# Optimization experiments

Hardware: AMD Instinct MI355X
Metric: run time of the kernel (lower is better)

The kernel has to match this reference:

```python
import jax, jax.numpy as jnp
import numpy as np

B, L, H = 4, 512, 768          # batch, seq_len, bert hidden
S, R = 100, 100                # num candidate spans, num relation pairs
E = 128                        # size embedding dim
TE, TR = 8, 6                  # entity / relation types
MAX_ENT_LEN = 100
NEG = -1e20


def _span_masks(rng, b, n, seq_len, max_len):
    # contiguous span masks with lengths in [1, max_len-1] so sum(-1) < max_len
    starts = rng.integers(0, seq_len - 1, size=(b, n))
    lengths = rng.integers(1, max_len, size=(b, n))
    ends = np.minimum(starts + lengths, seq_len)
    pos = np.arange(seq_len)
    m = (pos[None, None, :] >= starts[..., None]) & (pos[None, None, :] < ends[..., None])
    return jnp.asarray(m.astype(np.int32))


def setup_inputs() -> dict:
    rng = np.random.default_rng(0)
    key = jax.random.key(0)
    k = jax.random.split(key, 6)
    return {
        "last_hidden_state": jax.random.normal(k[0], (B, L, H), jnp.float32),
        "entity_mask": _span_masks(rng, B, S, L, MAX_ENT_LEN),
        "relations": jnp.asarray(rng.integers(0, S, size=(B, R, 2)).astype(np.int32)),
        "relation_context_mask": _span_masks(rng, B, R, L, MAX_ENT_LEN),
        "relation_sample_mask": jnp.asarray(rng.integers(0, 2, size=(B, R)).astype(np.int32)),
        "size_emb": jax.random.normal(k[1], (MAX_ENT_LEN, E), jnp.float32) * 0.02,
        "span_w": jax.random.normal(k[2], (E + 2 * H, TE), jnp.float32) * 0.02,
        "span_b": jnp.zeros((TE,), jnp.float32),
        "rel_w": jax.random.normal(k[3], (2 * E + 3 * H, TR), jnp.float32) * 0.02,
        "rel_b": jnp.zeros((TR,), jnp.float32),
    }


def _masked_max(h, mask):
    # h: [B,L,H], mask: [B,N,L] int {0,1} -> [B,N,H]
    mf = mask[..., None].astype(h.dtype)                       # [B,N,L,1]
    masked = jnp.where(mf == 0, jnp.asarray(NEG, h.dtype), h[:, None] * mf)
    return masked.max(axis=2)


def reference(last_hidden_state, entity_mask, relations, relation_context_mask,
              relation_sample_mask, size_emb, span_w, span_b, rel_w, rel_b):
    b = last_hidden_state.shape[0]
    # ---- entity classification ----
    context = last_hidden_state[:, 0]                          # CLS pooling [B,H]
    entity_size = size_emb[entity_mask.sum(-1)]                # [B,S,E]
    entity = _masked_max(last_hidden_state, entity_mask)       # [B,S,H]
    ctx = jnp.broadcast_to(context[:, None], (b, entity.shape[1], context.shape[-1]))
    entity_repr = jnp.concatenate([entity, ctx, entity_size], axis=-1)
    entity_logit = entity_repr @ span_w + span_b               # [B,S,TE]
    # ---- relation classification ----
    rel_ctx = _masked_max(last_hidden_state, relation_context_mask)  # [B,R,H]
    rel_ctx = jnp.where(relation_sample_mask[..., None] == 1,
                        jnp.zeros((), rel_ctx.dtype), rel_ctx)
    r = relations.shape[1]
    flat = relations.reshape(b, r * 2)                         # [B,2R]
    pair = jnp.take_along_axis(entity, flat[..., None], axis=1).reshape(b, r, -1)      # [B,R,2H]
    pair_size = jnp.take_along_axis(entity_size, flat[..., None], axis=1).reshape(b, r, -1)  # [B,R,2E]
    relation_repr = jnp.concatenate([rel_ctx, pair, pair_size], axis=-1)
    relation_logit = relation_repr @ rel_w + rel_b             # [B,R,TR]
    return entity_logit, relation_logit
```

## Files before the change

kernel.cpp:

```cpp
#include <hip/hip_runtime.h>

#define Bn 4
#define Ln 512
#define Hn 768
#define Sn 100
#define Rn 100
#define En 128
#define TEn 8
#define TRn 6
#define NEGF (-1e20f)
#define CHUNKS 3

__global__ void __launch_bounds__(256)
masked_max_kernel(const float* __restrict__ hid,
                  const int* __restrict__ ent_mask,
                  const int* __restrict__ rel_mask,
                  const int* __restrict__ sample_mask,
                  float* __restrict__ entity,
                  float* __restrict__ relctx,
                  int* __restrict__ entcnt) {
    int blk = blockIdx.x;
    int span_id = blk / CHUNKS;
    int chunk = blk % CHUNKS;
    int b = span_id / (Sn + Rn);
    int idx = span_id % (Sn + Rn);
    bool is_rel = idx >= Sn;
    int span = is_rel ? idx - Sn : idx;

    const int* mask = is_rel ? rel_mask + ((size_t)b * Rn + span) * Ln
                             : ent_mask + ((size_t)b * Sn + span) * Ln;

    __shared__ int pos[Ln];
    __shared__ int cnt_s;
    int tid = threadIdx.x;
    if (tid == 0) cnt_s = 0;
    __syncthreads();
    #pragma unroll
    for (int l = tid; l < Ln; l += 256) {
        if (mask[l] != 0) {
            int p = atomicAdd(&cnt_s, 1);
            pos[p] = l;
        }
    }
    __syncthreads();
    int cnt = cnt_s;

    int d = chunk * 256 + tid;
    const float* hp = hid + (size_t)b * Ln * Hn + d;
    float* out = is_rel ? relctx + ((size_t)b * Rn + span) * Hn
                        : entity + ((size_t)b * Sn + span) * Hn;
    bool zero_out = is_rel && (sample_mask[b * Rn + span] == 1);

    float m = NEGF;
    int i = 0;
    for (; i + 4 <= cnt; i += 4) {
        float v0 = hp[(size_t)pos[i + 0] * Hn];
        float v1 = hp[(size_t)pos[i + 1] * Hn];
        float v2 = hp[(size_t)pos[i + 2] * Hn];
        float v3 = hp[(size_t)pos[i + 3] * Hn];
        m = fmaxf(m, fmaxf(fmaxf(v0, v1), fmaxf(v2, v3)));
    }
    for (; i < cnt; ++i)
        m = fmaxf(m, hp[(size_t)pos[i] * Hn]);

    out[d] = zero_out ? 0.0f : m;
    if (chunk == 0 && !is_rel && tid == 0) entcnt[b * Sn + span] = cnt;
}

template <int NT>
__device__ __forceinline__ void block_reduce_store(float* acc,
                                                   const float* __restrict__ bias,
                                                   float* __restrict__ out_row,
                                                   int tid) {
    #pragma unroll
    for (int t = 0; t < NT; ++t)
        #pragma unroll
        for (int off = 32; off > 0; off >>= 1)
            acc[t] += __shfl_down(acc[t], off, 64);
    __shared__ float red[4][NT];
    int wave = tid >> 6, lane = tid & 63;
    if (lane == 0) {
        #pragma unroll
        for (int t = 0; t < NT; ++t) red[wave][t] = acc[t];
    }
    __syncthreads();
    if (tid < NT) {
        float s = bias[tid];
        #pragma unroll
        for (int w = 0; w < 4; ++w) s += red[w][tid];
        out_row[tid] = s;
    }
}

__global__ void __launch_bounds__(256)
logits_kernel(const float* __restrict__ hid,
              const float* __restrict__ entity,
              const float* __restrict__ relctx,
              const int* __restrict__ relations,
              const int* __restrict__ entcnt,
              const float* __restrict__ size_emb,
              const float* __restrict__ span_w,
              const float* __restrict__ span_b,
              const float* __restrict__ rel_w,
              const float* __restrict__ rel_b,
              float* __restrict__ out_ent,
              float* __restrict__ out_rel) {
    int blk = blockIdx.x;
    int tid = threadIdx.x;

    if (blk < Bn * Sn) {
        int b = blk / Sn;
        const float* ent = entity + (size_t)blk * Hn;
        const float* ctx = hid + (size_t)b * Ln * Hn;
        const float* sz = size_emb + (size_t)entcnt[blk] * En;

        float acc[TEn];
        #pragma unroll
        for (int t = 0; t < TEn; ++t) acc[t] = 0.0f;

        const int K = 2 * Hn + En;
        for (int k = tid; k < K; k += 256) {
            float v;
            if (k < Hn)          v = ent[k];
            else if (k < 2 * Hn) v = ctx[k - Hn];
            else                 v = sz[k - 2 * Hn];
            const float* w = span_w + (size_t)k * TEn;
            #pragma unroll
            for (int t = 0; t < TEn; ++t) acc[t] += v * w[t];
        }
        block_reduce_store<TEn>(acc, span_b, out_ent + (size_t)blk * TEn, tid);
    } else {
        int rblk = blk - Bn * Sn;
        int b = rblk / Rn;
        int a0 = relations[rblk * 2 + 0];
        int a1 = relations[rblk * 2 + 1];
        const float* ctx = relctx + (size_t)rblk * Hn;
        const float* e0 = entity + ((size_t)b * Sn + a0) * Hn;
        const float* e1 = entity + ((size_t)b * Sn + a1) * Hn;
        const float* s0 = size_emb + (size_t)entcnt[b * Sn + a0] * En;
        const float* s1 = size_emb + (size_t)entcnt[b * Sn + a1] * En;

        float acc[TRn];
        #pragma unroll
        for (int t = 0; t < TRn; ++t) acc[t] = 0.0f;

        const int K = 3 * Hn + 2 * En;
        for (int k = tid; k < K; k += 256) {
            float v;
            if (k < Hn)               v = ctx[k];
            else if (k < 2 * Hn)      v = e0[k - Hn];
            else if (k < 3 * Hn)      v = e1[k - 2 * Hn];
            else if (k < 3 * Hn + En) v = s0[k - 3 * Hn];
            else                      v = s1[k - 3 * Hn - En];
            const float* w = rel_w + (size_t)k * TRn;
            #pragma unroll
            for (int t = 0; t < TRn; ++t) acc[t] += v * w[t];
        }
        block_reduce_store<TRn>(acc, rel_b, out_rel + (size_t)rblk * TRn, tid);
    }
}

extern "C" void kernel_launch(void* const* d_in, const int* in_sizes, int n_in,
                              void* d_out, int out_size, void* d_ws, size_t ws_size,
                              hipStream_t stream) {
    const float* hid        = (const float*)d_in[0];
    const int*   ent_mask   = (const int*)d_in[1];
    const int*   relations  = (const int*)d_in[2];
    const int*   rel_mask   = (const int*)d_in[3];
    const int*   samp_mask  = (const int*)d_in[4];
    const float* size_emb   = (const float*)d_in[5];
    const float* span_w     = (const float*)d_in[6];
    const float* span_b     = (const float*)d_in[7];
    const float* rel_w      = (const float*)d_in[8];
    const float* rel_b      = (const float*)d_in[9];

    float* out = (float*)d_out;
    float* out_ent = out;
    float* out_rel = out + Bn * Sn * TEn;

    char* ws = (char*)d_ws;
    float* entity = (float*)ws;
    float* relctx = entity + (size_t)Bn * Sn * Hn;
    int*   entcnt = (int*)(relctx + (size_t)Bn * Rn * Hn);

    masked_max_kernel<<<Bn * (Sn + Rn) * CHUNKS, 256, 0, stream>>>(
        hid, ent_mask, rel_mask, samp_mask, entity, relctx, entcnt);

    logits_kernel<<<Bn * Sn + Bn * Rn, 256, 0, stream>>>(
        hid, entity, relctx, relations, entcnt, size_emb,
        span_w, span_b, rel_w, rel_b, out_ent, out_rel);
}
```

Baseline: 24.26 us.

## Precompute 8-row block maxima and vectorize masked max and logits loads

Adds a pre-pass kernel that computes the max over every aligned 8-row block of the hidden states. The masked-max kernel then combines fully covered blocks from this table and reads individual rows only at span edges, which cuts the number of rows gathered per span. It also uses float4 loads with one 192-thread block per span, and returns early for relation rows whose sample mask zeroes them. The logits kernel switches to vectorized activation and weight loads; the cost is an extra kernel launch and a workspace write.

```diff
diff --git a/kernel.cpp b/kernel.cpp
--- a/kernel.cpp
+++ b/kernel.cpp
@@ -9,62 +9,108 @@
 #define TEn 8
 #define TRn 6
 #define NEGF (-1e20f)
-#define CHUNKS 3
-
-__global__ void __launch_bounds__(256)
+#define W 8
+#define NBLK (Ln / W)
+#define H4 (Hn / 4)
+
+__device__ __forceinline__ float4 fmax4(float4 a, float4 b) {
+    return make_float4(fmaxf(a.x, b.x), fmaxf(a.y, b.y),
+                       fmaxf(a.z, b.z), fmaxf(a.w, b.w));
+}
+
+__global__ void __launch_bounds__(192)
+blockmax_kernel(const float* __restrict__ hid, float* __restrict__ bmax) {
+    int bj = blockIdx.x;
+    int b = bj / NBLK, j = bj % NBLK;
+    int tid = threadIdx.x;
+    const float4* src = (const float4*)(hid + ((size_t)b * Ln + j * W) * Hn);
+    float4 m = src[tid];
+    #pragma unroll
+    for (int r = 1; r < W; ++r)
+        m = fmax4(m, src[(size_t)r * H4 + tid]);
+    ((float4*)(bmax + (size_t)bj * Hn))[tid] = m;
+}
+
+__global__ void __launch_bounds__(192)
 masked_max_kernel(const float* __restrict__ hid,
                   const int* __restrict__ ent_mask,
                   const int* __restrict__ rel_mask,
                   const int* __restrict__ sample_mask,
+                  const float* __restrict__ bmax,
                   float* __restrict__ entity,
                   float* __restrict__ relctx,
                   int* __restrict__ entcnt) {
-    int blk = blockIdx.x;
-    int span_id = blk / CHUNKS;
-    int chunk = blk % CHUNKS;
+    int span_id = blockIdx.x;
     int b = span_id / (Sn + Rn);
     int idx = span_id % (Sn + Rn);
     bool is_rel = idx >= Sn;
     int span = is_rel ? idx - Sn : idx;
+    int tid = threadIdx.x;
+
+    float4* out4 = (float4*)(is_rel ? relctx + ((size_t)b * Rn + span) * Hn
+                                    : entity + ((size_t)b * Sn + span) * Hn);
+
+    if (is_rel && sample_mask[b * Rn + span] == 1) {
+        out4[tid] = make_float4(0.f, 0.f, 0.f, 0.f);
+        return;
+    }
 
     const int* mask = is_rel ? rel_mask + ((size_t)b * Rn + span) * Ln
                              : ent_mask + ((size_t)b * Sn + span) * Ln;
 
-    __shared__ int pos[Ln];
-    __shared__ int cnt_s;
-    int tid = threadIdx.x;
-    if (tid == 0) cnt_s = 0;
+    __shared__ int rows[Ln];
+    __shared__ int blks[NBLK];
+    __shared__ int nrows_s, nblks_s, cnt_s;
+    if (tid == 0) { nrows_s = 0; nblks_s = 0; }
     __syncthreads();
-    #pragma unroll
-    for (int l = tid; l < Ln; l += 256) {
-        if (mask[l] != 0) {
-            int p = atomicAdd(&cnt_s, 1);
-            pos[p] = l;
+
+    int local = 0;
+    if (tid < NBLK) {
+        const int4* m4 = (const int4*)(mask + tid * W);
+        int4 a = m4[0], c = m4[1];
+        int mm[8] = {a.x, a.y, a.z, a.w, c.x, c.y, c.z, c.w};
+        int s = 0;
+        #pragma unroll
+        for (int r = 0; r < 8; ++r) s += (mm[r] != 0);
+        local = s;
+        if (s == 8) {
+            int p = atomicAdd(&nblks_s, 1);
+            blks[p] = tid;
+        } else if (s > 0) {
+            #pragma unroll
+            for (int r = 0; r < 8; ++r)
+                if (mm[r] != 0) { int p = atomicAdd(&nrows_s, 1); rows[p] = tid * W + r; }
         }
+        #pragma unroll
+        for (int off = 32; off > 0; off >>= 1) local += __shfl_down(local, off, 64);
+        if (tid == 0) cnt_s = local;
     }
     __syncthreads();
-    int cnt = cnt_s;
-
-    int d = chunk * 256 + tid;
-    const float* hp = hid + (size_t)b * Ln * Hn + d;
-    float* out = is_rel ? relctx + ((size_t)b * Rn + span) * Hn
-                        : entity + ((size_t)b * Sn + span) * Hn;
-    bool zero_out = is_rel && (sample_mask[b * Rn + span] == 1);
-
-    float m = NEGF;
+    int nrows = nrows_s, nblks = nblks_s, cnt = cnt_s;
+
+    const float4* hb4 = (const float4*)(hid + (size_t)b * Ln * Hn);
+    const float4* bm4 = (const float4*)(bmax + (size_t)b * NBLK * Hn);
+
+    float4 m = make_float4(NEGF, NEGF, NEGF, NEGF);
     int i = 0;
-    for (; i + 4 <= cnt; i += 4) {
-        float v0 = hp[(size_t)pos[i + 0] * Hn];
-        float v1 = hp[(size_t)pos[i + 1] * Hn];
-        float v2 = hp[(size_t)pos[i + 2] * Hn];
-        float v3 = hp[(size_t)pos[i + 3] * Hn];
-        m = fmaxf(m, fmaxf(fmaxf(v0, v1), fmaxf(v2, v3)));
-    }
-    for (; i < cnt; ++i)
-        m = fmaxf(m, hp[(size_t)pos[i] * Hn]);
-
-    out[d] = zero_out ? 0.0f : m;
-    if (chunk == 0 && !is_rel && tid == 0) entcnt[b * Sn + span] = cnt;
+    for (; i + 2 <= nblks; i += 2) {
+        float4 v0 = bm4[(size_t)blks[i] * H4 + tid];
+        float4 v1 = bm4[(size_t)blks[i + 1] * H4 + tid];
+        m = fmax4(m, fmax4(v0, v1));
+    }
+    for (; i < nblks; ++i)
+        m = fmax4(m, bm4[(size_t)blks[i] * H4 + tid]);
+    i = 0;
+    for (; i + 2 <= nrows; i += 2) {
+        float4 v0 = hb4[(size_t)rows[i] * H4 + tid];
+        float4 v1 = hb4[(size_t)rows[i + 1] * H4 + tid];
+        m = fmax4(m, fmax4(v0, v1));
+    }
+    for (; i < nrows; ++i)
+        m = fmax4(m, hb4[(size_t)rows[i] * H4 + tid]);
+
+    out4[tid] = m;
+    if (!is_rel && tid == 0) entcnt[b * Sn + span] = cnt;
 }
 
 template <int NT>
@@ -110,23 +156,31 @@
 
     if (blk < Bn * Sn) {
         int b = blk / Sn;
-        const float* ent = entity + (size_t)blk * Hn;
-        const float* ctx = hid + (size_t)b * Ln * Hn;
-        const float* sz = size_emb + (size_t)entcnt[blk] * En;
+        const float4* ent4 = (const float4*)(entity + (size_t)blk * Hn);
+        const float4* ctx4 = (const float4*)(hid + (size_t)b * Ln * Hn);
+        const float4* sz4  = (const float4*)(size_emb + (size_t)entcnt[blk] * En);
 
         float acc[TEn];
         #pragma unroll
         for (int t = 0; t < TEn; ++t) acc[t] = 0.0f;
 
-        const int K = 2 * Hn + En;
-        for (int k = tid; k < K; k += 256) {
-            float v;
-            if (k < Hn)          v = ent[k];
-            else if (k < 2 * Hn) v = ctx[k - Hn];
-            else                 v = sz[k - 2 * Hn];
-            const float* w = span_w + (size_t)k * TEn;
+        const int K4 = (2 * Hn + En) / 4;
+        for (int k4 = tid; k4 < K4; k4 += 256) {
+            float4 v;
+            if (k4 < H4)          v = ent4[k4];
+            else if (k4 < 2 * H4) v = ctx4[k4 - H4];
+            else                  v = sz4[k4 - 2 * H4];
+            int k = k4 * 4;
+            const float4* w4 = (const float4*)(span_w + (size_t)k * TEn);
+            const float* vv = &v.x;
             #pragma unroll
-            for (int t = 0; t < TEn; ++t) acc[t] += v * w[t];
+            for (int j = 0; j < 4; ++j) {
+                float4 wa = w4[j * 2], wb = w4[j * 2 + 1];
+                acc[0] += vv[j] * wa.x; acc[1] += vv[j] * wa.y;
+                acc[2] += vv[j] * wa.z; acc[3] += vv[j] * wa.w;
+                acc[4] += vv[j] * wb.x; acc[5] += vv[j] * wb.y;
+                acc[6] += vv[j] * wb.z; acc[7] += vv[j] * wb.w;
+            }
         }
         block_reduce_store<TEn>(acc, span_b, out_ent + (size_t)blk * TEn, tid);
     } else {
@@ -134,27 +188,35 @@
         int b = rblk / Rn;
         int a0 = relations[rblk * 2 + 0];
         int a1 = relations[rblk * 2 + 1];
-        const float* ctx = relctx + (size_t)rblk * Hn;
-        const float* e0 = entity + ((size_t)b * Sn + a0) * Hn;
-        const float* e1 = entity + ((size_t)b * Sn + a1) * Hn;
-        const float* s0 = size_emb + (size_t)entcnt[b * Sn + a0] * En;
-        const float* s1 = size_emb + (size_t)entcnt[b * Sn + a1] * En;
+        const float4* ctx4 = (const float4*)(relctx + (size_t)rblk * Hn);
+        const float4* e04  = (const float4*)(entity + ((size_t)b * Sn + a0) * Hn);
+        const float4* e14  = (const float4*)(entity + ((size_t)b * Sn + a1) * Hn);
+        const float4* s04  = (const float4*)(size_emb + (size_t)entcnt[b * Sn + a0] * En);
+        const float4* s14  = (const float4*)(size_emb + (size_t)entcnt[b * Sn + a1] * En);
 
         float acc[TRn];
         #pragma unroll
         for (int t = 0; t < TRn; ++t) acc[t] = 0.0f;
 
-        const int K = 3 * Hn + 2 * En;
-        for (int k = tid; k < K; k += 256) {
-            float v;
-            if (k < Hn)               v = ctx[k];
-            else if (k < 2 * Hn)      v = e0[k - Hn];
-            else if (k < 3 * Hn)      v = e1[k - 2 * Hn];
-            else if (k < 3 * Hn + En) v = s0[k - 3 * Hn];
-            else                      v = s1[k - 3 * Hn - En];
-            const float* w = rel_w + (size_t)k * TRn;
+        const int E4 = En / 4;
+        const int K4 = (3 * Hn + 2 * En) / 4;
+        for (int k4 = tid; k4 < K4; k4 += 256) {
+            float4 v;
+            if (k4 < H4)               v = ctx4[k4];
+            else if (k4 < 2 * H4)      v = e04[k4 - H4];
+            else if (k4 < 3 * H4)      v = e14[k4 - 2 * H4];
+            else if (k4 < 3 * H4 + E4) v = s04[k4 - 3 * H4];
+            else                       v = s14[k4 - 3 * H4 - E4];
+            int k = k4 * 4;
+            const float* vv = &v.x;
             #pragma unroll
-            for (int t = 0; t < TRn; ++t) acc[t] += v * w[t];
+            for (int j = 0; j < 4; ++j) {
+                const float2* wr = (const float2*)(rel_w + (size_t)(k + j) * TRn);
+                float2 w0 = wr[0], w1 = wr[1], w2 = wr[2];
+                acc[0] += vv[j] * w0.x; acc[1] += vv[j] * w0.y;
+                acc[2] += vv[j] * w1.x; acc[3] += vv[j] * w1.y;
+                acc[4] += vv[j] * w2.x; acc[5] += vv[j] * w2.y;
+            }
         }
         block_reduce_store<TRn>(acc, rel_b, out_rel + (size_t)rblk * TRn, tid);
     }
@@ -181,10 +243,13 @@
     char* ws = (char*)d_ws;
     float* entity = (float*)ws;
     float* relctx = entity + (size_t)Bn * Sn * Hn;
-    int*   entcnt = (int*)(relctx + (size_t)Bn * Rn * Hn);
-
-    masked_max_kernel<<<Bn * (Sn + Rn) * CHUNKS, 256, 0, stream>>>(
-        hid, ent_mask, rel_mask, samp_mask, entity, relctx, entcnt);
+    float* bmax   = relctx + (size_t)Bn * Rn * Hn;
+    int*   entcnt = (int*)(bmax + (size_t)Bn * NBLK * Hn);
+
+    blockmax_kernel<<<Bn * NBLK, 192, 0, stream>>>(hid, bmax);
+
+    masked_max_kernel<<<Bn * (Sn + Rn), 192, 0, stream>>>(
+        hid, ent_mask, rel_mask, samp_mask, bmax, entity, relctx, entcnt);
 
     logits_kernel<<<Bn * Sn + Bn * Rn, 256, 0, stream>>>(
         hid, entity, relctx, relations, entcnt, size_emb,
```

Result: faster. 23.71 us (-2.3%).
